# Kernel tuning notes

Hardware: AMD Instinct MI355X
Metric: run time of the kernel (lower is better)

## Reference

```python
import jax, jax.numpy as jnp
import numpy as np

B, S, V, E, U, L = 32, 256, 32000, 512, 512, 2

def setup_inputs() -> dict:
    key = jax.random.key(0)
    ks = jax.random.split(key, 16)
    def p(k, shape, scale):
        return jax.random.normal(k, shape, dtype=jnp.float32) * scale
    inp = {
        "x": jax.random.randint(ks[0], (B, S), 0, V),
        "state": jnp.zeros((2 * L, B, U), jnp.float32),
        "emb_table": p(ks[1], (V, E), 0.05),
    }
    names = ["fk0", "frk0", "fb0", "fk1", "frk1", "fb1",
             "bk0", "brk0", "bb0", "bk1", "brk1", "bb1"]
    i = 2
    for n in names:
        if n.endswith("b0") or n.endswith("b1"):
            inp[n] = jnp.zeros((2, 3 * U), jnp.float32)
        else:
            inp[n] = p(ks[i], (512, 3 * U), 1.0 / np.sqrt(512))
        i += 1
    return inp

def gru_step(h, xt, k, rk, b):
    # TF2 GRUCell, reset_after=True
    mx = xt @ k + b[0]
    mi = h @ rk + b[1]
    xz, xr, xh = jnp.split(mx, 3, axis=-1)
    iz, ir, ih = jnp.split(mi, 3, axis=-1)
    z = jax.nn.sigmoid(xz + iz)
    r = jax.nn.sigmoid(xr + ir)
    hh = jnp.tanh(xh + r * ih)
    return z * h + (1.0 - z) * hh

def run_rnn(emb_s, mask_s, h0s, params):
    # emb_s: [S,B,E], mask_s: [S,B], h0s: tuple of L x [B,U]
    def step(carry, inp):
        hs, prev = carry
        xt, mt = inp
        m = mt[:, None]
        new_hs = []
        a = xt
        for h, (k, rk, b) in zip(hs, params):
            hn = gru_step(h, a, k, rk, b)
            hn = jnp.where(m, hn, h)  # masked steps carry state
            new_hs.append(hn)
            a = hn
        out = jnp.where(m, a, prev)  # masked steps repeat prev output
        return (tuple(new_hs), out), out
    init = (tuple(h0s), jnp.zeros((emb_s.shape[1], U), emb_s.dtype))
    (hs_f, _), ys = jax.lax.scan(step, init, (emb_s, mask_s))
    return ys, hs_f

def reference(x, state, emb_table,
              fk0, frk0, fb0, fk1, frk1, fb1,
              bk0, brk0, bb0, bk1, brk1, bb1):
    emb = emb_table[x]                      # [B,S,E]
    mask = (x != 0)                         # mask_zero=True
    emb_s = jnp.swapaxes(emb, 0, 1)         # [S,B,E]
    mask_s = jnp.swapaxes(mask, 0, 1)       # [S,B]
    fw_params = [(fk0, frk0, fb0), (fk1, frk1, fb1)]
    bw_params = [(bk0, brk0, bb0), (bk1, brk1, bb1)]
    ys_f, hs_f = run_rnn(emb_s, mask_s, (state[0], state[1]), fw_params)
    ys_b, hs_b = run_rnn(emb_s[::-1], mask_s[::-1], (state[2], state[3]), bw_params)
    ys_b = ys_b[::-1]
    y = jnp.concatenate([ys_f, ys_b], axis=-1)   # [S,B,2U]
    y = jnp.swapaxes(y, 0, 1)                    # [B,S,2U]
    states = jnp.stack(list(hs_f) + list(hs_b), axis=0)  # [2L,B,U]
    return y, states
```

## Files before the change

### kernel.cpp

```cpp
#include <hip/hip_runtime.h>
#include <hip/hip_bf16.h>

#define S_LEN 256
#define NB 32
#define UDIM 512
#define WGS 32
#define NH 16

typedef __attribute__((ext_vector_type(8))) short bf16x8;
typedef __attribute__((ext_vector_type(4))) float f32x4;
typedef __attribute__((ext_vector_type(4))) unsigned u32x4;

struct WPtrs { const float* p[8]; };
struct BPtrs { const float* p[4]; };

__device__ __forceinline__ unsigned short f2bf(float f) {
  union { float f; unsigned u; } v; v.f = f;
  unsigned r = v.u + 0x7fffu + ((v.u >> 16) & 1u);
  return (unsigned short)(r >> 16);
}

__device__ __forceinline__ int ld_flag(const int* p) {
  int v;
  asm volatile("global_load_dword %0, %1, off sc0 sc1\n\ts_waitcnt vmcnt(0)"
               : "=&v"(v) : "v"(p) : "memory");
  return v;
}
__device__ __forceinline__ void st_u32c(unsigned* p, unsigned v) {
  asm volatile("global_store_dword %0, %1, off sc0 sc1" :: "v"(p), "v"(v) : "memory");
}
__device__ __forceinline__ void st_flag(int* p, int v) {
  asm volatile("global_store_dword %0, %1, off sc0 sc1" :: "v"(p), "v"(v) : "memory");
}
__device__ __forceinline__ void ld_hist16(const short* p0, const short* p1,
                                          bf16x8* afr0, bf16x8* afr1) {
  u32x4 q0,q1,q2,q3,q4,q5,q6,q7,q8,q9,q10,q11,q12,q13,q14,q15;
  asm volatile(
    "global_load_dwordx4 %0, %16, off sc0 sc1\n\t"
    "global_load_dwordx4 %1, %16, off offset:64 sc0 sc1\n\t"
    "global_load_dwordx4 %2, %16, off offset:128 sc0 sc1\n\t"
    "global_load_dwordx4 %3, %16, off offset:192 sc0 sc1\n\t"
    "global_load_dwordx4 %4, %16, off offset:256 sc0 sc1\n\t"
    "global_load_dwordx4 %5, %16, off offset:320 sc0 sc1\n\t"
    "global_load_dwordx4 %6, %16, off offset:384 sc0 sc1\n\t"
    "global_load_dwordx4 %7, %16, off offset:448 sc0 sc1\n\t"
    "global_load_dwordx4 %8, %17, off sc0 sc1\n\t"
    "global_load_dwordx4 %9, %17, off offset:64 sc0 sc1\n\t"
    "global_load_dwordx4 %10, %17, off offset:128 sc0 sc1\n\t"
    "global_load_dwordx4 %11, %17, off offset:192 sc0 sc1\n\t"
    "global_load_dwordx4 %12, %17, off offset:256 sc0 sc1\n\t"
    "global_load_dwordx4 %13, %17, off offset:320 sc0 sc1\n\t"
    "global_load_dwordx4 %14, %17, off offset:384 sc0 sc1\n\t"
    "global_load_dwordx4 %15, %17, off offset:448 sc0 sc1\n\t"
    "s_waitcnt vmcnt(0)"
    : "=&v"(q0),"=&v"(q1),"=&v"(q2),"=&v"(q3),"=&v"(q4),"=&v"(q5),"=&v"(q6),"=&v"(q7),
      "=&v"(q8),"=&v"(q9),"=&v"(q10),"=&v"(q11),"=&v"(q12),"=&v"(q13),"=&v"(q14),"=&v"(q15)
    : "v"(p0), "v"(p1)
    : "memory");
  union U { u32x4 u; bf16x8 b; } cv;
  cv.u=q0;  afr0[0]=cv.b; cv.u=q1;  afr0[1]=cv.b; cv.u=q2;  afr0[2]=cv.b; cv.u=q3;  afr0[3]=cv.b;
  cv.u=q4;  afr0[4]=cv.b; cv.u=q5;  afr0[5]=cv.b; cv.u=q6;  afr0[6]=cv.b; cv.u=q7;  afr0[7]=cv.b;
  cv.u=q8;  afr1[0]=cv.b; cv.u=q9;  afr1[1]=cv.b; cv.u=q10; afr1[2]=cv.b; cv.u=q11; afr1[3]=cv.b;
  cv.u=q12; afr1[4]=cv.b; cv.u=q13; afr1[5]=cv.b; cv.u=q14; afr1[6]=cv.b; cv.u=q15; afr1[7]=cv.b;
}

__global__ void k_embed(const int* __restrict__ x, const float* __restrict__ tab,
                        unsigned short* __restrict__ emb, int* __restrict__ mask) {
  int t = blockIdx.x, b = blockIdx.y;
  int tok = x[b * S_LEN + t];
  if (threadIdx.x == 0) mask[t * NB + b] = (tok != 0);
  const float4* src = (const float4*)(tab + (size_t)tok * UDIM);
  ushort4* dst = (ushort4*)(emb + ((size_t)t * NB + b) * UDIM);
  int i = threadIdx.x;
  float4 v = src[i];
  ushort4 o;
  o.x = f2bf(v.x); o.y = f2bf(v.y); o.z = f2bf(v.z); o.w = f2bf(v.w);
  dst[i] = o;
}

__global__ void k_wprep(WPtrs wp, unsigned short* __restrict__ wsW) {
  int bid = blockIdx.x;
  int kt = bid & 31; bid >>= 5;
  int g  = bid % 3;  bid /= 3;
  int wg = bid & 31; bid >>= 5;
  int slab = bid;
  const float* src = wp.p[slab];
  int tid = threadIdx.x;
  int r = tid >> 4, cc = tid & 15;
  __shared__ float ldsT[16][17];
  ldsT[cc][r] = src[(size_t)(kt * 16 + r) * 1536 + g * 512 + wg * 16 + cc];
  __syncthreads();
  size_t off = ((size_t)slab * WGS + wg) * (48 * 512) + (size_t)(g * 16 + r) * 512 + kt * 16 + cc;
  wsW[off] = f2bf(ldsT[r][cc]);
}

__global__ __launch_bounds__(256, 1) void k_rnn(
    const unsigned short* __restrict__ wsW, const unsigned short* __restrict__ emb,
    unsigned short* __restrict__ hist, const int* __restrict__ mask,
    int* __restrict__ flags, const float* __restrict__ state,
    BPtrs bp, float* __restrict__ out) {
  __shared__ short sW[2 * 48 * 512];
  __shared__ float sAcc[2][2][32][48];
  __shared__ float sBias[2][48];
  __shared__ unsigned char sMask[S_LEN][NB];

  int tid = threadIdx.x;
  int bid = blockIdx.x;
  int xcd = bid & 7;
  int c = xcd >> 1;
  int w = ((bid >> 3) << 1) | (xcd & 1);
  int layer = c & 1;
  bool back = (c >= 2);
  int lane = tid & 63;
  int wave = tid >> 6;
  int mat = wave & 1;
  int kh = wave >> 1;

  int cb = tid >> 3;
  int cj = (tid & 7) << 1;
  float hreg0, hreg1, preg0 = 0.f, preg1 = 0.f;

  {
    const size_t slabSz = 48 * 512;
    for (int ch = tid; ch < 2 * 48 * 64; ch += 256) {
      int m = ch / (48 * 64);
      int rem = ch % (48 * 64);
      int nl = rem >> 6;
      int k16 = rem & 63;
      const unsigned short* sp =
          wsW + ((size_t)((c * 2 + m) * WGS) + w) * slabSz + (size_t)nl * 512 + k16 * 8;
      bf16x8 val = *(const bf16x8*)sp;
      int byte = m * 49152 + nl * 1024 + ((k16 * 16) ^ ((nl & 7) << 4));
      *(bf16x8*)((char*)sW + byte) = val;
    }
    const float* bptr = bp.p[c];
    for (int i = tid; i < 96; i += 256) {
      int m = i / 48, nl = i % 48;
      int col = (nl / 16) * 512 + w * 16 + (nl & 15);
      sBias[m][nl] = bptr[m * 1536 + col];
    }
    for (int i = tid; i < S_LEN * NB; i += 256)
      sMask[i >> 5][i & 31] = (unsigned char)(mask[i] != 0);
    int col = w * 16 + cj;
    hreg0 = state[((size_t)c * NB + cb) * UDIM + col];
    hreg1 = state[((size_t)c * NB + cb) * UDIM + col + 1];
    unsigned pk = (unsigned)f2bf(hreg0) | ((unsigned)f2bf(hreg1) << 16);
    st_u32c((unsigned*)(hist + (((size_t)c * 257) * NB + cb) * UDIM + col), pk);
  }
  asm volatile("s_waitcnt vmcnt(0)" ::: "memory");
  __syncthreads();
  if (tid == 0) st_flag(&flags[(c * 257) * 32 + w], 1);

  for (int t = 0; t < S_LEN; ++t) {
    int treal = back ? (S_LEN - 1 - t) : t;
    const unsigned short* arow;
    const int* fl = nullptr;
    int ownIdx = -1;
    if (mat == 0) {
      if (layer == 0) {
        arow = emb + (size_t)treal * NB * UDIM;
      } else {
        arow = hist + ((size_t)(c - 1) * 257 + (t + 1)) * NB * UDIM;
        fl = flags + ((c - 1) * 257 + (t + 1)) * 32;
      }
    } else {
      arow = hist + ((size_t)c * 257 + t) * NB * UDIM;
      fl = flags + (c * 257 + t) * 32;
      ownIdx = w;
    }

    int r15 = lane & 15, quad = lane >> 4;
    const short* a16 = (const short*)arow;
    int abase = r15 * UDIM + kh * 256 + quad * 8;

    bf16x8 afr0[8], afr1[8];
    if (fl) {
      const int* fp = fl + (lane & 31);
      bool sub = ((lane & 31) == ownIdx);
      int v = sub ? 1 : ld_flag(fp);
      while (!__all(v != 0)) {
        v = sub ? 1 : ld_flag(fp);
      }
      ld_hist16((const short*)(a16 + abase), (const short*)(a16 + abase + 16 * UDIM),
                afr0, afr1);
    } else {
#pragma unroll
      for (int kc = 0; kc < 8; ++kc) {
        afr0[kc] = *(const bf16x8*)(a16 + abase + kc * 32);
        afr1[kc] = *(const bf16x8*)(a16 + abase + 16 * UDIM + kc * 32);
      }
    }

    f32x4 acc[2][3];
#pragma unroll
    for (int a = 0; a < 2; a++)
#pragma unroll
      for (int g = 0; g < 3; g++) acc[a][g] = (f32x4){0.f, 0.f, 0.f, 0.f};
    int matbase = mat * 49152;
#pragma unroll
    for (int kc = 0; kc < 8; ++kc) {
#pragma unroll
      for (int g = 0; g < 3; ++g) {
        int nl = g * 16 + r15;
        int koff = kh * 512 + kc * 64 + quad * 16;
        int byte = matbase + nl * 1024 + (koff ^ ((nl & 7) << 4));
        bf16x8 bw = *(const bf16x8*)((const char*)sW + byte);
        acc[0][g] = __builtin_amdgcn_mfma_f32_16x16x32_bf16(afr0[kc], bw, acc[0][g], 0, 0, 0);
        acc[1][g] = __builtin_amdgcn_mfma_f32_16x16x32_bf16(afr1[kc], bw, acc[1][g], 0, 0, 0);
      }
    }
#pragma unroll
    for (int mt = 0; mt < 2; ++mt)
#pragma unroll
      for (int g = 0; g < 3; ++g)
#pragma unroll
        for (int rr = 0; rr < 4; ++rr)
          sAcc[kh][mat][mt * 16 + quad * 4 + rr][g * 16 + r15] = acc[mt][g][rr];
    __syncthreads();

    float hn0, hn1, o0, o1;
    bool mk;
    {
      int b = cb, j0 = cj;
      mk = sMask[treal][b] != 0;
#pragma unroll
      for (int u = 0; u < 2; ++u) {
        int j = j0 + u;
        float az = sAcc[0][0][b][j]      + sAcc[1][0][b][j]      + sBias[0][j];
        float ar = sAcc[0][0][b][16 + j] + sAcc[1][0][b][16 + j] + sBias[0][16 + j];
        float ah = sAcc[0][0][b][32 + j] + sAcc[1][0][b][32 + j] + sBias[0][32 + j];
        float iz = sAcc[0][1][b][j]      + sAcc[1][1][b][j]      + sBias[1][j];
        float ir = sAcc[0][1][b][16 + j] + sAcc[1][1][b][16 + j] + sBias[1][16 + j];
        float ih = sAcc[0][1][b][32 + j] + sAcc[1][1][b][32 + j] + sBias[1][32 + j];
        float z = 1.f / (1.f + __expf(-(az + iz)));
        float r = 1.f / (1.f + __expf(-(ar + ir)));
        float pre = ah + r * ih;
        pre = fminf(fmaxf(pre, -30.f), 30.f);
        float e2 = __expf(2.f * pre);
        float hh = (e2 - 1.f) / (e2 + 1.f);
        float hold = (u == 0) ? hreg0 : hreg1;
        float hv = z * hold + (1.f - z) * hh;
        hv = mk ? hv : hold;
        if (u == 0) hn0 = hv; else hn1 = hv;
      }
      hreg0 = hn0; hreg1 = hn1;
      unsigned pk = (unsigned)f2bf(hn0) | ((unsigned)f2bf(hn1) << 16);
      st_u32c((unsigned*)(hist + (((size_t)c * 257 + (t + 1)) * NB + cb) * UDIM + w * 16 + j0), pk);
    }
    asm volatile("s_waitcnt vmcnt(0)" ::: "memory");
    __syncthreads();
    if (tid == 0) st_flag(&flags[(c * 257 + (t + 1)) * 32 + w], 1);

    if (layer == 1) {
      o0 = mk ? hn0 : preg0;
      o1 = mk ? hn1 : preg1;
      preg0 = o0; preg1 = o1;
      *(float2*)(out + ((size_t)cb * S_LEN + treal) * 1024 + (back ? 512 : 0) + w * 16 + cj) =
          make_float2(o0, o1);
    }
    if (t == S_LEN - 1) {
      *(float2*)(out + (size_t)NB * S_LEN * 1024 + ((size_t)c * NB + cb) * UDIM + w * 16 + cj) =
          make_float2(hn0, hn1);
    }
  }
}

extern "C" void kernel_launch(void* const* d_in, const int* in_sizes, int n_in,
                              void* d_out, int out_size, void* d_ws, size_t ws_size,
                              hipStream_t stream) {
  const int* x = (const int*)d_in[0];
  const float* state = (const float*)d_in[1];
  const float* tab = (const float*)d_in[2];
  WPtrs wp;
  wp.p[0] = (const float*)d_in[3];
  wp.p[1] = (const float*)d_in[4];
  wp.p[2] = (const float*)d_in[6];
  wp.p[3] = (const float*)d_in[7];
  wp.p[4] = (const float*)d_in[9];
  wp.p[5] = (const float*)d_in[10];
  wp.p[6] = (const float*)d_in[12];
  wp.p[7] = (const float*)d_in[13];
  BPtrs bp;
  bp.p[0] = (const float*)d_in[5];
  bp.p[1] = (const float*)d_in[8];
  bp.p[2] = (const float*)d_in[11];
  bp.p[3] = (const float*)d_in[14];
  float* out = (float*)d_out;

  char* ws = (char*)d_ws;
  size_t off = 0;
  unsigned short* wsW = (unsigned short*)(ws + off); off += (size_t)8 * 32 * 48 * 512 * 2;
  unsigned short* embp = (unsigned short*)(ws + off); off += (size_t)S_LEN * NB * UDIM * 2;
  unsigned short* hist = (unsigned short*)(ws + off); off += (size_t)4 * 257 * NB * UDIM * 2;
  int* maskp = (int*)(ws + off); off += (size_t)S_LEN * NB * 4;
  int* flags = (int*)(ws + off); off += (size_t)4 * 257 * 32 * 4;

  hipMemsetAsync(flags, 0, (size_t)4 * 257 * 32 * 4, stream);
  k_embed<<<dim3(S_LEN, NB), 128, 0, stream>>>(x, tab, embp, maskp);
  k_wprep<<<8 * 32 * 3 * 32, 256, 0, stream>>>(wp, wsW);
  k_rnn<<<128, 256, 0, stream>>>(wsW, embp, hist, maskp, flags, state, bp, out);
}
```

Before: 1.130 ms.

## Drop store waits before flag publish and validate history with sentinel fill

```diff
diff --git a/kernel.cpp b/kernel.cpp
--- a/kernel.cpp
+++ b/kernel.cpp
@@ -5,7 +5,7 @@
 #define NB 32
 #define UDIM 512
 #define WGS 32
-#define NH 16
+#define FPAD 32
 
 typedef __attribute__((ext_vector_type(8))) short bf16x8;
 typedef __attribute__((ext_vector_type(4))) float f32x4;
@@ -32,7 +32,8 @@
 __device__ __forceinline__ void st_flag(int* p, int v) {
   asm volatile("global_store_dword %0, %1, off sc0 sc1" :: "v"(p), "v"(v) : "memory");
 }
-__device__ __forceinline__ void ld_hist16(const short* p0, const short* p1,
+
+__device__ __forceinline__ bool ld_hist16(const short* p0, const short* p1,
                                           bf16x8* afr0, bf16x8* afr1) {
   u32x4 q0,q1,q2,q3,q4,q5,q6,q7,q8,q9,q10,q11,q12,q13,q14,q15;
   asm volatile(
@@ -57,11 +58,18 @@
       "=&v"(q8),"=&v"(q9),"=&v"(q10),"=&v"(q11),"=&v"(q12),"=&v"(q13),"=&v"(q14),"=&v"(q15)
     : "v"(p0), "v"(p1)
     : "memory");
+  const unsigned S = 0xFFFFFFFFu;
+  bool bad = false;
+#define CK(q) bad |= (q[0]==S)|(q[1]==S)|(q[2]==S)|(q[3]==S)
+  CK(q0);CK(q1);CK(q2);CK(q3);CK(q4);CK(q5);CK(q6);CK(q7);
+  CK(q8);CK(q9);CK(q10);CK(q11);CK(q12);CK(q13);CK(q14);CK(q15);
+#undef CK
   union U { u32x4 u; bf16x8 b; } cv;
   cv.u=q0;  afr0[0]=cv.b; cv.u=q1;  afr0[1]=cv.b; cv.u=q2;  afr0[2]=cv.b; cv.u=q3;  afr0[3]=cv.b;
   cv.u=q4;  afr0[4]=cv.b; cv.u=q5;  afr0[5]=cv.b; cv.u=q6;  afr0[6]=cv.b; cv.u=q7;  afr0[7]=cv.b;
   cv.u=q8;  afr1[0]=cv.b; cv.u=q9;  afr1[1]=cv.b; cv.u=q10; afr1[2]=cv.b; cv.u=q11; afr1[3]=cv.b;
   cv.u=q12; afr1[4]=cv.b; cv.u=q13; afr1[5]=cv.b; cv.u=q14; afr1[6]=cv.b; cv.u=q15; afr1[7]=cv.b;
+  return !bad;
 }
 
 __global__ void k_embed(const int* __restrict__ x, const float* __restrict__ tab,
@@ -100,7 +108,7 @@
     int* __restrict__ flags, const float* __restrict__ state,
     BPtrs bp, float* __restrict__ out) {
   __shared__ short sW[2 * 48 * 512];
-  __shared__ float sAcc[2][2][32][48];
+  __shared__ float sAcc[2][2][2][32][48];
   __shared__ float sBias[2][48];
   __shared__ unsigned char sMask[S_LEN][NB];
 
@@ -147,11 +155,15 @@
     unsigned pk = (unsigned)f2bf(hreg0) | ((unsigned)f2bf(hreg1) << 16);
     st_u32c((unsigned*)(hist + (((size_t)c * 257) * NB + cb) * UDIM + col), pk);
   }
-  asm volatile("s_waitcnt vmcnt(0)" ::: "memory");
   __syncthreads();
-  if (tid == 0) st_flag(&flags[(c * 257) * 32 + w], 1);
+  if (tid == 0) st_flag(&flags[((c * 257) * 32 + w) * FPAD], 1);
+
+  int r15 = lane & 15, quad = lane >> 4;
+  int abase = r15 * UDIM + kh * 256 + quad * 8;
+  int matbase = mat * 49152;
 
   for (int t = 0; t < S_LEN; ++t) {
+    int par = t & 1;
     int treal = back ? (S_LEN - 1 - t) : t;
     const unsigned short* arow;
     const int* fl = nullptr;
@@ -161,34 +173,32 @@
         arow = emb + (size_t)treal * NB * UDIM;
       } else {
         arow = hist + ((size_t)(c - 1) * 257 + (t + 1)) * NB * UDIM;
-        fl = flags + ((c - 1) * 257 + (t + 1)) * 32;
+        fl = flags + ((c - 1) * 257 + (t + 1)) * 32 * FPAD;
       }
     } else {
       arow = hist + ((size_t)c * 257 + t) * NB * UDIM;
-      fl = flags + (c * 257 + t) * 32;
+      fl = flags + (c * 257 + t) * 32 * FPAD;
       ownIdx = w;
     }
 
-    int r15 = lane & 15, quad = lane >> 4;
     const short* a16 = (const short*)arow;
-    int abase = r15 * UDIM + kh * 256 + quad * 8;
+    const short* p0 = a16 + abase;
+    const short* p1 = p0 + 16 * UDIM;
 
     bf16x8 afr0[8], afr1[8];
     if (fl) {
-      const int* fp = fl + (lane & 31);
+      const int* fp = fl + (lane & 31) * FPAD;
       bool sub = ((lane & 31) == ownIdx);
       int v = sub ? 1 : ld_flag(fp);
-      while (!__all(v != 0)) {
-        v = sub ? 1 : ld_flag(fp);
+      while (!__all(v != 0)) v = sub ? 1 : ld_flag(fp);
+      bool ok = ld_hist16(p0, p1, afr0, afr1);
+      while (!__all(ok)) ok = ld_hist16(p0, p1, afr0, afr1);
+    } else {
+#pragma unroll
+      for (int kc = 0; kc < 8; ++kc) {
+        afr0[kc] = *(const bf16x8*)(p0 + kc * 32);
+        afr1[kc] = *(const bf16x8*)(p1 + kc * 32);
       }
-      ld_hist16((const short*)(a16 + abase), (const short*)(a16 + abase + 16 * UDIM),
-                afr0, afr1);
-    } else {
-#pragma unroll
-      for (int kc = 0; kc < 8; ++kc) {
-        afr0[kc] = *(const bf16x8*)(a16 + abase + kc * 32);
-        afr1[kc] = *(const bf16x8*)(a16 + abase + 16 * UDIM + kc * 32);
-      }
     }
 
     f32x4 acc[2][3];
@@ -196,7 +206,6 @@
     for (int a = 0; a < 2; a++)
 #pragma unroll
       for (int g = 0; g < 3; g++) acc[a][g] = (f32x4){0.f, 0.f, 0.f, 0.f};
-    int matbase = mat * 49152;
 #pragma unroll
     for (int kc = 0; kc < 8; ++kc) {
 #pragma unroll
@@ -215,10 +224,10 @@
       for (int g = 0; g < 3; ++g)
 #pragma unroll
         for (int rr = 0; rr < 4; ++rr)
-          sAcc[kh][mat][mt * 16 + quad * 4 + rr][g * 16 + r15] = acc[mt][g][rr];
+          sAcc[par][kh][mat][mt * 16 + quad * 4 + rr][g * 16 + r15] = acc[mt][g][rr];
     __syncthreads();
 
-    float hn0, hn1, o0, o1;
+    float hn0, hn1;
     bool mk;
     {
       int b = cb, j0 = cj;
@@ -226,12 +235,12 @@
 #pragma unroll
       for (int u = 0; u < 2; ++u) {
         int j = j0 + u;
-        float az = sAcc[0][0][b][j]      + sAcc[1][0][b][j]      + sBias[0][j];
-        float ar = sAcc[0][0][b][16 + j] + sAcc[1][0][b][16 + j] + sBias[0][16 + j];
-        float ah = sAcc[0][0][b][32 + j] + sAcc[1][0][b][32 + j] + sBias[0][32 + j];
-        float iz = sAcc[0][1][b][j]      + sAcc[1][1][b][j]      + sBias[1][j];
-        float ir = sAcc[0][1][b][16 + j] + sAcc[1][1][b][16 + j] + sBias[1][16 + j];
-        float ih = sAcc[0][1][b][32 + j] + sAcc[1][1][b][32 + j] + sBias[1][32 + j];
+        float az = sAcc[par][0][0][b][j]      + sAcc[par][1][0][b][j]      + sBias[0][j];
+        float ar = sAcc[par][0][0][b][16 + j] + sAcc[par][1][0][b][16 + j] + sBias[0][16 + j];
+        float ah = sAcc[par][0][0][b][32 + j] + sAcc[par][1][0][b][32 + j] + sBias[0][32 + j];
+        float iz = sAcc[par][0][1][b][j]      + sAcc[par][1][1][b][j]      + sBias[1][j];
+        float ir = sAcc[par][0][1][b][16 + j] + sAcc[par][1][1][b][16 + j] + sBias[1][16 + j];
+        float ih = sAcc[par][0][1][b][32 + j] + sAcc[par][1][1][b][32 + j] + sBias[1][32 + j];
         float z = 1.f / (1.f + __expf(-(az + iz)));
         float r = 1.f / (1.f + __expf(-(ar + ir)));
         float pre = ah + r * ih;
@@ -247,13 +256,12 @@
       unsigned pk = (unsigned)f2bf(hn0) | ((unsigned)f2bf(hn1) << 16);
       st_u32c((unsigned*)(hist + (((size_t)c * 257 + (t + 1)) * NB + cb) * UDIM + w * 16 + j0), pk);
     }
-    asm volatile("s_waitcnt vmcnt(0)" ::: "memory");
-    __syncthreads();
-    if (tid == 0) st_flag(&flags[(c * 257 + (t + 1)) * 32 + w], 1);
+    __builtin_amdgcn_s_barrier();
+    if (tid == 0) st_flag(&flags[((c * 257 + (t + 1)) * 32 + w) * FPAD], 1);
 
     if (layer == 1) {
-      o0 = mk ? hn0 : preg0;
-      o1 = mk ? hn1 : preg1;
+      float o0 = mk ? hn0 : preg0;
+      float o1 = mk ? hn1 : preg1;
       preg0 = o0; preg1 = o1;
       *(float2*)(out + ((size_t)cb * S_LEN + treal) * 1024 + (back ? 512 : 0) + w * 16 + cj) =
           make_float2(o0, o1);
@@ -291,11 +299,14 @@
   size_t off = 0;
   unsigned short* wsW = (unsigned short*)(ws + off); off += (size_t)8 * 32 * 48 * 512 * 2;
   unsigned short* embp = (unsigned short*)(ws + off); off += (size_t)S_LEN * NB * UDIM * 2;
-  unsigned short* hist = (unsigned short*)(ws + off); off += (size_t)4 * 257 * NB * UDIM * 2;
+  unsigned short* hist = (unsigned short*)(ws + off);
+  size_t histBytes = (size_t)4 * 257 * NB * UDIM * 2;  off += histBytes;
   int* maskp = (int*)(ws + off); off += (size_t)S_LEN * NB * 4;
-  int* flags = (int*)(ws + off); off += (size_t)4 * 257 * 32 * 4;
-
-  hipMemsetAsync(flags, 0, (size_t)4 * 257 * 32 * 4, stream);
+  int* flags = (int*)(ws + off);
+  size_t flagBytes = (size_t)4 * 257 * 32 * FPAD * 4;  off += flagBytes;
+
+  hipMemsetAsync(hist, 0xFF, histBytes, stream);
+  hipMemsetAsync(flags, 0, flagBytes, stream);
   k_embed<<<dim3(S_LEN, NB), 128, 0, stream>>>(x, tab, embp, maskp);
   k_wprep<<<8 * 32 * 3 * 32, 256, 0, stream>>>(wp, wsW);
   k_rnn<<<128, 256, 0, stream>>>(wsW, embp, hist, maskp, flags, state, bp, out);
```

New measurement: 1.123 ms. No clear change (-0.6%).
